# Optimization experiments

Measured on AMD Instinct MI355X. Metric: run time of the kernel, lower is better.

The kernel has to match this reference:

```python
import math
import jax, jax.numpy as jnp
import numpy as np

B, N, F = 4, 2048, 128
H, D = 8, 128  # num_heads, out_dim per head (out_dim == in_dim for residual)
EPS = 1e-5
NEG = -1e30  # finite stand-in for -inf; exp(NEG - rowmax) == 0 for any valid row


def setup_inputs() -> dict:
    key = jax.random.key(0)
    ks = jax.random.split(key, 10)
    x = jax.random.normal(ks[0], (B, N, F), dtype=jnp.float32)
    # sparse-ish graph adjacency mask + active-node mask
    attn_mask = jax.random.bernoulli(ks[1], 0.05, (B, N, N))
    # ensure self loops so most rows are non-empty (isolated-node nan path still exercised via node_mask)
    eye = jnp.eye(N, dtype=bool)[None]
    attn_mask = attn_mask | eye
    node_mask = jax.random.bernoulli(ks[2], 0.9, (B, N))
    s = 1.0 / math.sqrt(F)
    Wq = jax.random.normal(ks[3], (F, H * D), dtype=jnp.float32) * s
    Wk = jax.random.normal(ks[4], (F, H * D), dtype=jnp.float32) * s
    Wv = jax.random.normal(ks[5], (F, H * D), dtype=jnp.float32) * s
    Wo = jax.random.normal(ks[6], (H * D, D), dtype=jnp.float32) * (1.0 / math.sqrt(H * D))
    bo = jnp.zeros((D,), dtype=jnp.float32)
    gamma = jnp.ones((D,), dtype=jnp.float32)
    beta = jnp.zeros((D,), dtype=jnp.float32)
    return {"x": x, "attn_mask": attn_mask, "node_mask": node_mask,
            "Wq": Wq, "Wk": Wk, "Wv": Wv, "Wo": Wo, "bo": bo,
            "gamma": gamma, "beta": beta}


def reference(x, attn_mask, node_mask, Wq, Wk, Wv, Wo, bo, gamma, beta):
    # projections -> [B, H, N, D]
    q = (x @ Wq).reshape(B, N, H, D).transpose(0, 2, 1, 3)
    k = (x @ Wk).reshape(B, N, H, D).transpose(0, 2, 1, 3)
    v = (x @ Wv).reshape(B, N, H, D).transpose(0, 2, 1, 3)
    scores = jnp.einsum("bhnd,bhmd->bhnm", q, k) / math.sqrt(D)
    # pair_mask: adjacency (broadcast over heads) AND query-node validity
    pair_mask = attn_mask[:, None, :, :] & node_mask[:, None, :, None]  # [B,H(=1),N,N]
    scores = jnp.where(pair_mask, scores, NEG)
    attn = jax.nn.softmax(scores, axis=-1)
    # rows with no valid key (== torch's nan_to_num of all -inf softmax) -> zeros
    row_valid = pair_mask.any(axis=-1, keepdims=True)
    attn = jnp.where(row_valid, attn, 0.0)
    out = jnp.einsum("bhnm,bhmd->bhnd", attn, v)
    out = out.transpose(0, 2, 1, 3).reshape(B, N, H * D)
    out = out @ Wo + bo
    out = out + x  # residual (in_dim == out_dim)
    # LayerNorm over last dim
    mu = out.mean(axis=-1, keepdims=True)
    var = ((out - mu) ** 2).mean(axis=-1, keepdims=True)
    out = (out - mu) * jax.lax.rsqrt(var + EPS) * gamma + beta
    out = out * jax.nn.sigmoid(out)  # SiLU
    out = out * node_mask[..., None]
    return out
```

## Files before the change

kernel.cpp:

```cpp
#include <hip/hip_runtime.h>

#define NTOK 2048
#define NB 4
#define NH 8
#define DH 128

typedef __bf16 bf16x8 __attribute__((ext_vector_type(8)));
typedef unsigned short u16x8 __attribute__((ext_vector_type(8)));
typedef float f32x4 __attribute__((ext_vector_type(4)));
typedef float f32x16 __attribute__((ext_vector_type(16)));
typedef unsigned int u32x4 __attribute__((ext_vector_type(4)));

__device__ __forceinline__ f32x4 mfma16(bf16x8 a, bf16x8 b, f32x4 c) {
  return __builtin_amdgcn_mfma_f32_16x16x32_bf16(a, b, c, 0, 0, 0);
}
__device__ __forceinline__ f32x16 mfma32(bf16x8 a, bf16x8 b, f32x16 c) {
  return __builtin_amdgcn_mfma_f32_32x32x16_bf16(a, b, c, 0, 0, 0);
}
__device__ __forceinline__ bf16x8 ldb(const unsigned short* p) {
  return __builtin_bit_cast(bf16x8, *(const u16x8*)p);
}
__device__ __forceinline__ bf16x8 ldsb(const char* p) {
  return __builtin_bit_cast(bf16x8, *(const u16x8*)p);
}
__device__ __forceinline__ unsigned short f2bf(float f) {
  unsigned int u = __builtin_bit_cast(unsigned int, f);
  u += 0x7fffu + ((u >> 16) & 1u);
  return (unsigned short)(u >> 16);
}
__device__ __forceinline__ unsigned int cvtpk(float lo, float hi) {
  unsigned int r;
  asm("v_cvt_pk_bf16_f32 %0, %1, %2" : "=v"(r) : "v"(lo), "v"(hi));
  return r;
}
#if __has_builtin(__builtin_amdgcn_exp2f)
__device__ __forceinline__ float exp2a(float x) { return __builtin_amdgcn_exp2f(x); }
#else
__device__ __forceinline__ float exp2a(float x) { return __expf(x * 0.6931471805599453f); }
#endif
#define GLL(gsrc, ldst) __builtin_amdgcn_global_load_lds(                      \
    (const __attribute__((address_space(1))) void*)(gsrc),                     \
    (__attribute__((address_space(3))) void*)(ldst), 16, 0, 0)
#define WAITVM_(N) asm volatile("s_waitcnt vmcnt(" #N ")" ::: "memory")
#define WAITVM(N) WAITVM_(N)
#define SFENCE() asm volatile("" ::: "memory")

__device__ __forceinline__ bool mask_at(const void* p, int flag, int idx) {
  if (flag == 1) return ((const unsigned char*)p)[idx] != 0;
  return ((const int*)p)[idx] != 0;
}

__global__ __launch_bounds__(256) void k_prep(
    const float* __restrict__ x, const float* __restrict__ Wq,
    const float* __restrict__ Wk, const float* __restrict__ Wv,
    const float* __restrict__ Wo, const unsigned int* __restrict__ amdw,
    unsigned short* __restrict__ xb, unsigned short* __restrict__ wqt,
    unsigned short* __restrict__ wkt, unsigned short* __restrict__ wvt,
    unsigned short* __restrict__ wot, int* __restrict__ flag) {
  int bid = blockIdx.x, tid = threadIdx.x;
  if (bid == 0) {
    __shared__ int su8, sf32;
    if (tid == 0) { su8 = 0; sf32 = 0; }
    __syncthreads();
    const uint4* dw4 = (const uint4*)amdw;
    int lu8 = 0, lf32 = 0;
#pragma unroll
    for (int j = 0; j < 16; j++) {
      uint4 q = dw4[tid + j * 256];
      unsigned int vv[4] = {q.x, q.y, q.z, q.w};
#pragma unroll
      for (int e = 0; e < 4; e++) {
        unsigned int v = vv[e];
        if (v == 0x3f800000u) lf32 = 1;
        else if (v != 0u && v != 1u) lu8 = 1;
      }
    }
    if (lu8) atomicOr(&su8, 1);
    if (lf32) atomicOr(&sf32, 1);
    __syncthreads();
    if (tid == 0) *flag = sf32 ? 2 : (su8 ? 1 : 0);
    return;
  }
  if (bid < 513) {
    int base = (bid - 1) * 2048 + tid * 8;
    const float4* xf = (const float4*)(x + base);
    float4 a = xf[0], b = xf[1];
    u16x8 o;
    o[0] = f2bf(a.x); o[1] = f2bf(a.y); o[2] = f2bf(a.z); o[3] = f2bf(a.w);
    o[4] = f2bf(b.x); o[5] = f2bf(b.y); o[6] = f2bf(b.z); o[7] = f2bf(b.w);
    *(u16x8*)(xb + base) = o;
    return;
  }
  __shared__ float tile[64][65];
  int tb = bid - 513;
  int msel = tb >> 5, tt = tb & 31;
  const float* w; unsigned short* wt; int R, C;
  if (msel == 0)      { w = Wq; wt = wqt; R = 128;  C = 1024; }
  else if (msel == 1) { w = Wk; wt = wkt; R = 128;  C = 1024; }
  else if (msel == 2) { w = Wv; wt = wvt; R = 128;  C = 1024; }
  else                { w = Wo; wt = wot; R = 1024; C = 128; }
  int nrt = R >> 6;
  int rt = (tt % nrt) << 6, ct = (tt / nrt) << 6;
  {
    int cl = tid & 63, rg = tid >> 6;
#pragma unroll
    for (int j = 0; j < 16; j++) {
      int row = rg * 16 + j;
      tile[row][cl] = w[(size_t)(rt + row) * C + ct + cl];
    }
  }
  __syncthreads();
  {
    int rl = tid & 63, cg = tid >> 6;
#pragma unroll
    for (int j = 0; j < 16; j++) {
      int col = cg * 16 + j;
      wt[(size_t)(ct + col) * R + rt + rl] = f2bf(tile[rl][col]);
    }
  }
}

__global__ __launch_bounds__(256) void k_qkv_pack(
    const unsigned short* __restrict__ xb, const unsigned short* __restrict__ wqt,
    const unsigned short* __restrict__ wkt, const unsigned short* __restrict__ wvt,
    unsigned short* __restrict__ qb, unsigned short* __restrict__ kbuf,
    unsigned short* __restrict__ vtb, const void* __restrict__ am,
    const int* __restrict__ flagp, unsigned int* __restrict__ bits) {
  __shared__ char smem[49152];
  int bid = blockIdx.x;
  int lane = threadIdx.x & 63, w = threadIdx.x >> 6;
  if (bid >= 3072) {
    int flag = *flagp;
    size_t ebase = (size_t)(bid - 3072) * 8192 + (size_t)threadIdx.x * 32;
    unsigned int word = 0;
    if (flag == 1) {
      const uint4* p4 = (const uint4*)((const unsigned char*)am + ebase);
      uint4 q0 = p4[0], q1 = p4[1];
      unsigned int dw[8] = {q0.x, q0.y, q0.z, q0.w, q1.x, q1.y, q1.z, q1.w};
#pragma unroll
      for (int d = 0; d < 8; d++) {
        unsigned int v = dw[d];
        if (v & 0x000000FFu) word |= 1u << (d * 4 + 0);
        if (v & 0x0000FF00u) word |= 1u << (d * 4 + 1);
        if (v & 0x00FF0000u) word |= 1u << (d * 4 + 2);
        if (v & 0xFF000000u) word |= 1u << (d * 4 + 3);
      }
    } else {
      const uint4* p4 = (const uint4*)((const int*)am + ebase);
#pragma unroll
      for (int k = 0; k < 8; k++) {
        uint4 q = p4[k];
        if (q.x) word |= 1u << (k * 4 + 0);
        if (q.y) word |= 1u << (k * 4 + 1);
        if (q.z) word |= 1u << (k * 4 + 2);
        if (q.w) word |= 1u << (k * 4 + 3);
      }
    }
    bits[ebase >> 5] = word;
    return;
  }
  int which = bid >> 10;
  int rem = bid & 1023;
  int bx = rem & 127, by = rem >> 7;
  const unsigned short* wt = which == 0 ? wqt : (which == 1 ? wkt : wvt);
  int lo = lane & 15, g = lane >> 4;
  int rbase = bx * 64 + w * 16;
  int colb = by * 128;
  char* wl = smem;
  {
    const char* Wg = (const char*)(wt + (size_t)colb * 128);
#pragma unroll
    for (int s = 0; s < 8; s++) {
      int a = s * 4096 + w * 1024 + lane * 16;
      int r = a >> 8;
      int cb = (a & 255) ^ ((r & 7) << 4);
      GLL(Wg + r * 256 + cb, wl + s * 4096 + w * 1024);
    }
  }
  bf16x8 af[4];
  const unsigned short* xrow = xb + (size_t)(rbase + lo) * 128 + g * 8;
#pragma unroll
  for (int s = 0; s < 4; s++) af[s] = ldb(xrow + 32 * s);
  __syncthreads();
  f32x4 acc[8] = {};
  int xw = (lo & 7) << 4;
#pragma unroll
  for (int c = 0; c < 8; c++) {
    const char* wrow = wl + (c * 16 + lo) * 256;
#pragma unroll
    for (int s = 0; s < 4; s++)
      acc[c] = mfma16(af[s], ldsb(wrow + ((64 * s + 16 * g) ^ xw)), acc[c]);
  }
  if (which != 2) {
    float sc = (which == 0) ? 0.12751743f : 1.0f;
#pragma unroll
    for (int c = 0; c < 8; c++) {
#pragma unroll
      for (int r = 0; r < 4; r++) {
        int row = rbase + 4 * g + r;
        int col = colb + c * 16 + lo;
        int b = row >> 11, n = row & (NTOK - 1);
        int h = col >> 7, d = col & 127;
        unsigned short val = f2bf(acc[c][r] * sc);
        size_t bh = (size_t)(b * NH + h);
        if (which == 0) qb[(bh * NTOK + n) * DH + d] = val;
        else            kbuf[(bh * NTOK + n) * DH + d] = val;
      }
    }
    return;
  }
  unsigned short* vt_lds = (unsigned short*)(smem + 32768);
#pragma unroll
  for (int c = 0; c < 8; c++) {
#pragma unroll
    for (int r = 0; r < 4; r++) {
      int nl = w * 16 + 4 * g + r;
      int d = c * 16 + lo;
      int boff = d * 128 + ((nl * 2) ^ ((d & 7) << 4));
      *(unsigned short*)((char*)vt_lds + boff) = f2bf(acc[c][r]);
    }
  }
  __syncthreads();
  int t = threadIdx.x;
  int d = t >> 1, half = t & 1;
  int bb = (bx * 64) >> 11;
  int n0 = (bx * 64) & (NTOK - 1);
  size_t bh = (size_t)(bb * NH + by);
  unsigned short* dst = vtb + (bh * DH + d) * NTOK + n0 + half * 32;
  const char* srcb = (const char*)vt_lds + d * 128;
#pragma unroll
  for (int s = 0; s < 4; s++) {
    int lb = (half * 64 + s * 16) ^ ((d & 7) << 4);
    *(u16x8*)(dst + s * 8) = *(const u16x8*)(srcb + lb);
  }
}

__device__ __forceinline__ void stageK(const char* Kg, char* kl, int w, int lane) {
#pragma unroll
  for (int s = 0; s < 4; s++) {
    int a = s * 4096 + w * 1024 + lane * 16;
    int r = a >> 8;
    int cb = (a & 255) ^ ((r & 7) << 4);
    GLL(Kg + r * 256 + cb, kl + s * 4096 + w * 1024);
  }
}
__device__ __forceinline__ void stageV(const char* Vg, char* vl, int w, int lane) {
#pragma unroll
  for (int s = 0; s < 4; s++) {
    int a = s * 4096 + w * 1024 + lane * 16;
    int r = a >> 7;
    int cb = (a & 127) ^ ((r & 7) << 4);
    GLL(Vg + (size_t)r * (NTOK * 2) + cb, vl + s * 4096 + w * 1024);
  }
}

#define QKBLK(SC0, SC1, KC)                                                    \
  {                                                                            \
    _Pragma("unroll") for (int r_ = 0; r_ < 16; r_++) { SC0[r_] = 0.f; SC1[r_] = 0.f; } \
    const char* kr0_ = (KC) + ql * 256;                                        \
    const char* kr1_ = (KC) + (32 + ql) * 256;                                 \
    _Pragma("unroll")                                                          \
    for (int s_ = 0; s_ < 8; s_++) {                                           \
      int cb_ = (32 * s_ + 16 * hi) ^ xk;                                      \
      SC0 = mfma32(ldsb(kr0_ + cb_), qf[s_], SC0);                             \
      SC1 = mfma32(ldsb(kr1_ + cb_), qf[s_], SC1);                             \
    }                                                                          \
  }

#define SOFTPACK(SC0, SC1, MMV, PSV, FA0, FA1, FB0, FB1)                       \
  {                                                                            \
    unsigned int mw0_ = (MMV).x >> (4 * hi), mw1_ = (MMV).y >> (4 * hi);       \
    float sv0_[16], sv1_[16];                                                  \
    _Pragma("unroll")                                                          \
    for (int r_ = 0; r_ < 16; r_++) {                                          \
      int cp_ = (r_ & 3) + 8 * (r_ >> 2);                                      \
      sv0_[r_] = ((mw0_ >> cp_) & 1u) ? SC0[r_] : -3.0e38f;                    \
      sv1_[r_] = ((mw1_ >> cp_) & 1u) ? SC1[r_] : -3.0e38f;                    \
    }                                                                          \
    PSV = 0.f;                                                                 \
    _Pragma("unroll")                                                          \
    for (int r_ = 0; r_ < 16; r_++) { sv0_[r_] = exp2a(sv0_[r_] - m); PSV += sv0_[r_]; } \
    _Pragma("unroll")                                                          \
    for (int r_ = 0; r_ < 16; r_++) { sv1_[r_] = exp2a(sv1_[r_] - m); PSV += sv1_[r_]; } \
    unsigned int w8a_[8], w8b_[8], pa_[8], pb_[8];                             \
    _Pragma("unroll")                                                          \
    for (int j_ = 0; j_ < 8; j_++) {                                           \
      w8a_[j_] = cvtpk(sv0_[2 * j_], sv0_[2 * j_ + 1]);                        \
      w8b_[j_] = cvtpk(sv1_[2 * j_], sv1_[2 * j_ + 1]);                        \
    }                                                                          \
    _Pragma("unroll")                                                          \
    for (int j_ = 0; j_ < 8; j_++) {                                           \
      pa_[j_] = __shfl_xor((int)w8a_[j_], 32, 64);                             \
      pb_[j_] = __shfl_xor((int)w8b_[j_], 32, 64);                             \
    }                                                                          \
    u32x4 ta0_, ta1_, tb0_, tb1_;                                              \
    if (hi) {                                                                  \
      ta0_ = u32x4{pa_[2], pa_[3], w8a_[2], w8a_[3]};                          \
      ta1_ = u32x4{pa_[6], pa_[7], w8a_[6], w8a_[7]};                          \
      tb0_ = u32x4{pb_[2], pb_[3], w8b_[2], w8b_[3]};                          \
      tb1_ = u32x4{pb_[6], pb_[7], w8b_[6], w8b_[7]};                          \
    } else {                                                                   \
      ta0_ = u32x4{w8a_[0], w8a_[1], pa_[0], pa_[1]};                          \
      ta1_ = u32x4{w8a_[4], w8a_[5], pa_[4], pa_[5]};                          \
      tb0_ = u32x4{w8b_[0], w8b_[1], pb_[0], pb_[1]};                          \
      tb1_ = u32x4{w8b_[4], w8b_[5], pb_[4], pb_[5]};                          \
    }                                                                          \
    FA0 = __builtin_bit_cast(bf16x8, ta0_);                                    \
    FA1 = __builtin_bit_cast(bf16x8, ta1_);                                    \
    FB0 = __builtin_bit_cast(bf16x8, tb0_);                                    \
    FB1 = __builtin_bit_cast(bf16x8, tb1_);                                    \
  }

#define PVBLK(FA0, FA1, FB0, FB1, VC)                                          \
  {                                                                            \
    const char* vr0_ = (VC) + (ql + 0) * 128;                                  \
    const char* vr1_ = (VC) + (ql + 32) * 128;                                 \
    const char* vr2_ = (VC) + (ql + 64) * 128;                                 \
    const char* vr3_ = (VC) + (ql + 96) * 128;                                 \
    int c0_ = (16 * hi) ^ xk, c1_ = (32 + 16 * hi) ^ xk;                       \
    int c2_ = (64 + 16 * hi) ^ xk, c3_ = (96 + 16 * hi) ^ xk;                  \
    o0 = mfma32(FA0, ldsb(vr0_ + c0_), o0);                                    \
    o1 = mfma32(FA0, ldsb(vr1_ + c0_), o1);                                    \
    o2 = mfma32(FA0, ldsb(vr2_ + c0_), o2);                                    \
    o3 = mfma32(FA0, ldsb(vr3_ + c0_), o3);                                    \
    o0 = mfma32(FA1, ldsb(vr0_ + c1_), o0);                                    \
    o1 = mfma32(FA1, ldsb(vr1_ + c1_), o1);                                    \
    o2 = mfma32(FA1, ldsb(vr2_ + c1_), o2);                                    \
    o3 = mfma32(FA1, ldsb(vr3_ + c1_), o3);                                    \
    o0 = mfma32(FB0, ldsb(vr0_ + c2_), o0);                                    \
    o1 = mfma32(FB0, ldsb(vr1_ + c2_), o1);                                    \
    o2 = mfma32(FB0, ldsb(vr2_ + c2_), o2);                                    \
    o3 = mfma32(FB0, ldsb(vr3_ + c2_), o3);                                    \
    o0 = mfma32(FB1, ldsb(vr0_ + c3_), o0);                                    \
    o1 = mfma32(FB1, ldsb(vr1_ + c3_), o1);                                    \
    o2 = mfma32(FB1, ldsb(vr2_ + c3_), o2);                                    \
    o3 = mfma32(FB1, ldsb(vr3_ + c3_), o3);                                    \
  }

#define BIG(PSV)                                                               \
  if (__any((PSV) > 65536.0f)) {                                               \
    const float c_ = 1.52587890625e-05f;                                       \
    m += 16.0f; l *= c_;                                                       \
    _Pragma("unroll")                                                          \
    for (int r_ = 0; r_ < 16; r_++) { o0[r_] *= c_; o1[r_] *= c_; o2[r_] *= c_; o3[r_] *= c_; } \
  }

#define BODY(PI0, PI1, PI2, PI3, PSI, PO0, PO1, PO2, PO3, PSO, MMV)            \
  {                                                                            \
    __builtin_amdgcn_s_setprio(1);                                             \
    QKBLK(sT0, sT1, smem + ko_rd);                                             \
    PVBLK(PI0, PI1, PI2, PI3, smem + vo_pv);                                   \
    __builtin_amdgcn_s_setprio(0);                                             \
    l += PSI;                                                                  \
    BIG(PSI);                                                                  \
    SOFTPACK(sT0, sT1, MMV, PSO, PO0, PO1, PO2, PO3);                          \
  }

#define ROT_V() { int t_ = vo_pv; vo_pv = vo_mid; vo_mid = vo_st; vo_st = t_; }
#define SWAP_K() { int t_ = ko_rd; ko_rd = ko_nx; ko_nx = t_; }

#define TAIL(KT, VT, MMREG, MI)                                                \
  __builtin_amdgcn_s_barrier();                                                \
  stageK(Kbase + (size_t)(KT) * 16384, smem + ko_rd, w, lane);                 \
  stageV(Vbase + (size_t)(VT) * 128, smem + vo_st, w, lane);                   \
  SFENCE();                                                                    \
  MMREG = mrow[MI];                                                            \
  SFENCE();                                                                    \
  SWAP_K();                                                                    \
  ROT_V();

__global__ __launch_bounds__(256, 2) void k_attn64(
    const unsigned short* __restrict__ qb, const unsigned short* __restrict__ kbuf,
    const unsigned short* __restrict__ vtb, const unsigned int* __restrict__ mbits,
    unsigned short* __restrict__ aout) {
  __shared__ char smem[81920];
  int bid = blockIdx.x;
  int low3 = bid & 7, mid2 = (bid >> 3) & 3, qc = bid >> 5;
  int b = low3 >> 1, h = ((low3 & 1) << 2) | mid2;
  int bh = b * 8 + h;
  int lane = threadIdx.x & 63, w = threadIdx.x >> 6;
  int ql = lane & 31, hi = lane >> 5;
  int q0 = qc * 128 + w * 32;
  const char* Kbase = (const char*)(kbuf + (size_t)bh * NTOK * DH);
  const char* Vbase = (const char*)(vtb + (size_t)bh * NTOK * DH);
  int xk = (ql & 7) << 4;

  bf16x8 qf[8];
  {
    const unsigned short* qrow = qb + (size_t)bh * NTOK * DH + (size_t)(q0 + ql) * DH + 8 * hi;
#pragma unroll
    for (int s = 0; s < 8; s++) qf[s] = ldb(qrow + 16 * s);
  }
  const uint2* mrow = (const uint2*)(mbits + (size_t)b * (NTOK * NTOK / 32) + (size_t)(q0 + ql) * (NTOK / 32));
  SFENCE();
  uint2 mmB = mrow[0];
  uint2 mmA = mrow[1];
  SFENCE();
  stageK(Kbase, smem + 0, w, lane);
  stageK(Kbase + 16384, smem + 16384, w, lane);
  stageV(Vbase, smem + 32768, w, lane);
  SFENCE();

  int ko_rd = 0, ko_nx = 16384;
  int vo_pv = 65536, vo_mid = 32768, vo_st = 49152;
  f32x16 o0 = {}, o1 = {}, o2 = {}, o3 = {};
  f32x16 sT0, sT1;
  bf16x8 pE0, pE1, pE2, pE3, pO0, pO1, pO2, pO3;
  float psE = 0.f, psO = 0.f;
  float m = 0.0f, l = 0.0f;

  WAITVM(8); __builtin_amdgcn_s_barrier();
  QKBLK(sT0, sT1, smem + ko_rd);
  SOFTPACK(sT0, sT1, mmB, psE, pE0, pE1, pE2, pE3);
  TAIL(2, 1, mmB, 2);
  for (int tt = 1; tt <= 27; tt += 2) {
    WAITVM(9); __builtin_amdgcn_s_barrier();
    BODY(pE0, pE1, pE2, pE3, psE, pO0, pO1, pO2, pO3, psO, mmA);
    TAIL(tt + 2, tt + 1, mmA, tt + 2);
    WAITVM(9); __builtin_amdgcn_s_barrier();
    BODY(pO0, pO1, pO2, pO3, psO, pE0, pE1, pE2, pE3, psE, mmB);
    TAIL(tt + 3, tt + 2, mmB, tt + 3);
  }
  WAITVM(9); __builtin_amdgcn_s_barrier();
  BODY(pE0, pE1, pE2, pE3, psE, pO0, pO1, pO2, pO3, psO, mmA);
  TAIL(31, 30, mmA, 31);
  WAITVM(9); __builtin_amdgcn_s_barrier();
  BODY(pO0, pO1, pO2, pO3, psO, pE0, pE1, pE2, pE3, psE, mmB);
  __builtin_amdgcn_s_barrier();
  stageV(Vbase + (size_t)31 * 128, smem + vo_st, w, lane);
  SFENCE();
  SWAP_K();
  ROT_V();
  WAITVM(4); __builtin_amdgcn_s_barrier();
  BODY(pE0, pE1, pE2, pE3, psE, pO0, pO1, pO2, pO3, psO, mmA);
  ROT_V();
  WAITVM(0); __builtin_amdgcn_s_barrier();
  PVBLK(pO0, pO1, pO2, pO3, smem + vo_pv);
  l += psO;
  float lj = l + __shfl_xor(l, 32, 64);
  float linv = lj > 0.f ? 1.0f / lj : 0.0f;
  float li[16];
#pragma unroll
  for (int r = 0; r < 16; r++) {
    int qr = (r & 3) + 8 * (r >> 2) + 4 * hi;
    li[r] = __shfl(linv, qr, 64);
  }
  unsigned short* obase = aout + (size_t)b * NTOK * (NH * DH) + (size_t)h * DH + ql;
#pragma unroll
  for (int r = 0; r < 16; r++) {
    int qn = q0 + (r & 3) + 8 * (r >> 2) + 4 * hi;
    unsigned short* op = obase + (size_t)qn * (NH * DH);
    op[0]  = f2bf(o0[r] * li[r]);
    op[32] = f2bf(o1[r] * li[r]);
    op[64] = f2bf(o2[r] * li[r]);
    op[96] = f2bf(o3[r] * li[r]);
  }
}

__global__ __launch_bounds__(256) void k_gemm3(
    const unsigned short* __restrict__ aout, const unsigned short* __restrict__ wot,
    const float* __restrict__ x, const float* __restrict__ bo,
    const float* __restrict__ gamma, const float* __restrict__ beta,
    const void* __restrict__ nmask, const int* __restrict__ flagp,
    float* __restrict__ out) {
  __shared__ float red[4][16][132];
  int flag = *flagp;
  int lane = threadIdx.x & 63, w = threadIdx.x >> 6;
  int lo = lane & 15, g = lane >> 4;
  int rowb = blockIdx.x * 16;
  int k0 = w * 256;
  f32x4 acc[8] = {};
  const unsigned short* arow = aout + (size_t)(rowb + lo) * 1024 + k0 + g * 8;
#pragma unroll
  for (int ks = 0; ks < 8; ks++) {
    bf16x8 af = ldb(arow + 32 * ks);
#pragma unroll
    for (int t = 0; t < 8; t++) {
      bf16x8 bf = ldb(wot + (size_t)(t * 16 + lo) * 1024 + k0 + g * 8 + 32 * ks);
      acc[t] = mfma16(af, bf, acc[t]);
    }
  }
#pragma unroll
  for (int t = 0; t < 8; t++)
#pragma unroll
    for (int r = 0; r < 4; r++) red[w][4 * g + r][t * 16 + lo] = acc[t][r];
  __syncthreads();
  int row = threadIdx.x >> 4, cg = threadIdx.x & 15;
  float y[8];
#pragma unroll
  for (int j = 0; j < 8; j++) {
    int col = cg * 8 + j;
    y[j] = red[0][row][col] + red[1][row][col] + red[2][row][col] + red[3][row][col]
         + bo[col] + x[(size_t)(rowb + row) * 128 + col];
  }
  float s = 0.f;
#pragma unroll
  for (int j = 0; j < 8; j++) s += y[j];
  s += __shfl_xor(s, 1, 64); s += __shfl_xor(s, 2, 64);
  s += __shfl_xor(s, 4, 64); s += __shfl_xor(s, 8, 64);
  float mu = s * 0.0078125f;
  float vs = 0.f;
#pragma unroll
  for (int j = 0; j < 8; j++) { float d = y[j] - mu; vs += d * d; }
  vs += __shfl_xor(vs, 1, 64); vs += __shfl_xor(vs, 2, 64);
  vs += __shfl_xor(vs, 4, 64); vs += __shfl_xor(vs, 8, 64);
  float rstd = rsqrtf(vs * 0.0078125f + 1e-5f);
  float nm = mask_at(nmask, flag, rowb + row) ? 1.0f : 0.0f;
  float ov[8];
#pragma unroll
  for (int j = 0; j < 8; j++) {
    int col = cg * 8 + j;
    float z = (y[j] - mu) * rstd * gamma[col] + beta[col];
    z = z / (1.0f + __expf(-z));
    ov[j] = z * nm;
  }
  float* op = out + (size_t)(rowb + row) * 128 + cg * 8;
  *(float4*)op = float4{ov[0], ov[1], ov[2], ov[3]};
  *(float4*)(op + 4) = float4{ov[4], ov[5], ov[6], ov[7]};
}

extern "C" void kernel_launch(void* const* d_in, const int* in_sizes, int n_in,
                              void* d_out, int out_size, void* d_ws, size_t ws_size,
                              hipStream_t stream) {
  (void)in_sizes; (void)n_in; (void)out_size;
  const float* x = (const float*)d_in[0];
  const void* amask = d_in[1];
  const void* nmask = d_in[2];
  const float* Wq = (const float*)d_in[3];
  const float* Wk = (const float*)d_in[4];
  const float* Wv = (const float*)d_in[5];
  const float* Wo = (const float*)d_in[6];
  const float* bo = (const float*)d_in[7];
  const float* gamma = (const float*)d_in[8];
  const float* beta = (const float*)d_in[9];
  float* out = (float*)d_out;
  char* ws = (char*)d_ws;

  constexpr size_t OFF_FLAG = 0;
  constexpr size_t OFF_XB   = 256;
  constexpr size_t OFF_WQT  = OFF_XB  + (size_t)8192 * 128 * 2;
  constexpr size_t OFF_WKT  = OFF_WQT + (size_t)1024 * 128 * 2;
  constexpr size_t OFF_WVT  = OFF_WKT + (size_t)1024 * 128 * 2;
  constexpr size_t OFF_WOT  = OFF_WVT + (size_t)1024 * 128 * 2;
  constexpr size_t OFF_BITS = OFF_WOT + (size_t)1024 * 128 * 2;
  constexpr size_t OFF_QB   = OFF_BITS + (size_t)NB * NTOK * NTOK / 8;
  constexpr size_t OFF_KB   = OFF_QB  + (size_t)NB * NH * NTOK * DH * 2;
  constexpr size_t OFF_VTB  = OFF_KB  + (size_t)NB * NH * NTOK * DH * 2;
  constexpr size_t OFF_AO   = OFF_VTB + (size_t)NB * NH * NTOK * DH * 2;
  constexpr size_t TOTAL    = OFF_AO  + (size_t)NB * NTOK * NH * DH * 2;
  if (ws_size < TOTAL) return;

  int* flag = (int*)(ws + OFF_FLAG);
  unsigned short* xb  = (unsigned short*)(ws + OFF_XB);
  unsigned short* wqt = (unsigned short*)(ws + OFF_WQT);
  unsigned short* wkt = (unsigned short*)(ws + OFF_WKT);
  unsigned short* wvt = (unsigned short*)(ws + OFF_WVT);
  unsigned short* wot = (unsigned short*)(ws + OFF_WOT);
  unsigned int* bits  = (unsigned int*)(ws + OFF_BITS);
  unsigned short* qb  = (unsigned short*)(ws + OFF_QB);
  unsigned short* kbf = (unsigned short*)(ws + OFF_KB);
  unsigned short* vtb = (unsigned short*)(ws + OFF_VTB);
  unsigned short* ao  = (unsigned short*)(ws + OFF_AO);

  k_prep<<<641, 256, 0, stream>>>(x, Wq, Wk, Wv, Wo, (const unsigned int*)amask,
                                  xb, wqt, wkt, wvt, wot, flag);
  k_qkv_pack<<<5120, 256, 0, stream>>>(xb, wqt, wkt, wvt, qb, kbf, vtb,
                                       amask, flag, bits);
  k_attn64<<<512, 256, 0, stream>>>(qb, kbf, vtb, bits, ao);
  k_gemm3<<<512, 256, 0, stream>>>(ao, wot, x, bo, gamma, beta, nmask, flag, out);
}
```

Baseline: 137.0 us.

## Split attention over key halves with partial outputs and a combine kernel

Adds a split-KV attention kernel that processes 32-key tiles over half of the key range per block, doubling the grid to 1024 blocks. Each block writes fp32 partial outputs plus row sums and running max to workspace, and a new combine kernel merges the two halves and writes bf16 attention output. The aim is higher occupancy and more parallelism on the attention stage. The cost is extra fp32 partial traffic (about 64 MB written and read) and one more launch. The new path only runs when the workspace is large enough.

```diff
diff --git a/kernel.cpp b/kernel.cpp
--- a/kernel.cpp
+++ b/kernel.cpp
@@ -233,6 +233,162 @@
     int lb = (half * 64 + s * 16) ^ ((d & 7) << 4);
     *(u16x8*)(dst + s * 8) = *(const u16x8*)(srcb + lb);
   }
+}
+
+__device__ __forceinline__ void stageK32(const char* Kg, char* kl, int w, int lane) {
+#pragma unroll
+  for (int s = 0; s < 2; s++) {
+    int a = s * 4096 + w * 1024 + lane * 16;
+    int r = a >> 8;
+    int cb = (a & 255) ^ ((r & 7) << 4);
+    GLL(Kg + r * 256 + cb, kl + s * 4096 + w * 1024);
+  }
+}
+__device__ __forceinline__ void stageV32(const char* Vg, char* vl, int w, int lane) {
+#pragma unroll
+  for (int s = 0; s < 2; s++) {
+    int a = s * 4096 + w * 1024 + lane * 16;
+    int r = a >> 6;
+    int cb = (a & 63) ^ ((r & 3) << 4);
+    GLL(Vg + (size_t)r * (NTOK * 2) + cb, vl + s * 4096 + w * 1024);
+  }
+}
+
+__global__ __launch_bounds__(256, 4) void k_attn32s(
+    const unsigned short* __restrict__ qb, const unsigned short* __restrict__ kbuf,
+    const unsigned short* __restrict__ vtb, const unsigned int* __restrict__ mbits,
+    float* __restrict__ opart, float* __restrict__ lpart, float* __restrict__ mpart) {
+  __shared__ char smem[32768];
+  int bid = blockIdx.x;
+  int low3 = bid & 7, mid2 = (bid >> 3) & 3, split = (bid >> 5) & 1, qc = bid >> 6;
+  int b = low3 >> 1, h = ((low3 & 1) << 2) | mid2;
+  int bh = b * 8 + h;
+  int lane = threadIdx.x & 63, w = threadIdx.x >> 6;
+  int ql = lane & 31, hi = lane >> 5;
+  int q0 = qc * 128 + w * 32;
+  const char* Kg = (const char*)(kbuf + (size_t)bh * NTOK * DH) + (size_t)split * 1024 * 256;
+  const char* Vg = (const char*)(vtb + (size_t)bh * NTOK * DH) + (size_t)split * 2048;
+  int xk = (ql & 7) << 4;
+  int xv = (ql & 3) << 4;
+
+  bf16x8 qf[8];
+  {
+    const unsigned short* qrow = qb + (size_t)bh * NTOK * DH + (size_t)(q0 + ql) * DH + 8 * hi;
+#pragma unroll
+    for (int s = 0; s < 8; s++) qf[s] = ldb(qrow + 16 * s);
+  }
+  const unsigned int* mrow = mbits + (size_t)b * (NTOK * NTOK / 32)
+                           + (size_t)(q0 + ql) * (NTOK / 32) + split * 32;
+  char* kl = smem;
+  char* vl = smem + 16384;
+  stageK32(Kg, kl, w, lane);
+  stageV32(Vg, vl, w, lane);
+  __syncthreads();
+
+  f32x16 o0 = {}, o1 = {}, o2 = {}, o3 = {};
+  float m = 0.0f, l = 0.0f;
+  for (int kt = 0; kt < 32; kt++) {
+    int cur = kt & 1;
+    const char* kc = kl + cur * 8192;
+    const char* vc = vl + cur * 8192;
+    if (kt < 31) {
+      stageK32(Kg + (size_t)(kt + 1) * 8192, kl + (1 - cur) * 8192, w, lane);
+      stageV32(Vg + (size_t)(kt + 1) * 64, vl + (1 - cur) * 8192, w, lane);
+    }
+    unsigned int mword = mrow[kt];
+    f32x16 sT = {};
+    const char* kr = kc + ql * 256;
+#pragma unroll
+    for (int s = 0; s < 8; s++)
+      sT = mfma32(ldsb(kr + ((32 * s + 16 * hi) ^ xk)), qf[s], sT);
+    unsigned int mw = mword >> (4 * hi);
+    float sv[16];
+#pragma unroll
+    for (int r = 0; r < 16; r++) {
+      int cp = (r & 3) + 8 * (r >> 2);
+      sv[r] = ((mw >> cp) & 1u) ? sT[r] : -3.0e38f;
+    }
+    float ps = 0.f;
+#pragma unroll
+    for (int r = 0; r < 16; r++) { sv[r] = exp2a(sv[r] - m); ps += sv[r]; }
+    ps += __shfl_xor(ps, 32, 64);
+    l += ps;
+    unsigned int w8[8], pa[8];
+#pragma unroll
+    for (int j = 0; j < 8; j++) w8[j] = cvtpk(sv[2 * j], sv[2 * j + 1]);
+#pragma unroll
+    for (int j = 0; j < 8; j++) pa[j] = __shfl_xor((int)w8[j], 32, 64);
+    u32x4 t0, t1;
+    if (hi) {
+      t0 = u32x4{pa[2], pa[3], w8[2], w8[3]};
+      t1 = u32x4{pa[6], pa[7], w8[6], w8[7]};
+    } else {
+      t0 = u32x4{w8[0], w8[1], pa[0], pa[1]};
+      t1 = u32x4{w8[4], w8[5], pa[4], pa[5]};
+    }
+    bf16x8 fk0 = __builtin_bit_cast(bf16x8, t0);
+    bf16x8 fk1 = __builtin_bit_cast(bf16x8, t1);
+    {
+      const char* vr0 = vc + (ql + 0) * 64;
+      const char* vr1 = vc + (ql + 32) * 64;
+      const char* vr2 = vc + (ql + 64) * 64;
+      const char* vr3 = vc + (ql + 96) * 64;
+      int c0 = (16 * hi) ^ xv, c1 = (32 + 16 * hi) ^ xv;
+      o0 = mfma32(fk0, ldsb(vr0 + c0), o0);
+      o1 = mfma32(fk0, ldsb(vr1 + c0), o1);
+      o2 = mfma32(fk0, ldsb(vr2 + c0), o2);
+      o3 = mfma32(fk0, ldsb(vr3 + c0), o3);
+      o0 = mfma32(fk1, ldsb(vr0 + c1), o0);
+      o1 = mfma32(fk1, ldsb(vr1 + c1), o1);
+      o2 = mfma32(fk1, ldsb(vr2 + c1), o2);
+      o3 = mfma32(fk1, ldsb(vr3 + c1), o3);
+    }
+    if (__any(ps > 65536.0f)) {
+      const float c = 1.52587890625e-05f;
+      m += 16.0f; l *= c;
+#pragma unroll
+      for (int r = 0; r < 16; r++) { o0[r] *= c; o1[r] *= c; o2[r] *= c; o3[r] *= c; }
+    }
+    __syncthreads();
+  }
+  size_t prow = (size_t)split * (32 * NTOK) + (size_t)bh * NTOK;
+#pragma unroll
+  for (int r = 0; r < 16; r++) {
+    int q = q0 + (r & 3) + 8 * (r >> 2) + 4 * hi;
+    float* op = opart + (prow + q) * 128;
+    op[ql]      = o0[r];
+    op[32 + ql] = o1[r];
+    op[64 + ql] = o2[r];
+    op[96 + ql] = o3[r];
+  }
+  if (hi == 0) {
+    lpart[prow + q0 + ql] = l;
+    mpart[prow + q0 + ql] = m;
+  }
+}
+
+__global__ __launch_bounds__(256) void k_comb(
+    const float* __restrict__ opart, const float* __restrict__ lpart,
+    const float* __restrict__ mpart, unsigned short* __restrict__ aout) {
+  int idx = blockIdx.x * 256 + threadIdx.x;
+  int d4 = idx & 31;
+  int row = idx >> 5;
+  float l0 = lpart[row], l1 = lpart[65536 + row];
+  float m0 = mpart[row], m1 = mpart[65536 + row];
+  float M = fmaxf(m0, m1);
+  float w0 = exp2a(m0 - M), w1 = exp2a(m1 - M);
+  float den = l0 * w0 + l1 * w1;
+  float inv = den > 0.f ? 1.0f / den : 0.f;
+  float4 a = *((const float4*)(opart + (size_t)row * 128) + d4);
+  float4 c = *((const float4*)(opart + ((size_t)65536 + row) * 128) + d4);
+  ushort4 r;
+  r.x = f2bf((a.x * w0 + c.x * w1) * inv);
+  r.y = f2bf((a.y * w0 + c.y * w1) * inv);
+  r.z = f2bf((a.z * w0 + c.z * w1) * inv);
+  r.w = f2bf((a.w * w0 + c.w * w1) * inv);
+  int bh = row >> 11, q = row & (NTOK - 1);
+  int b = bh >> 3, h = bh & 7;
+  *(ushort4*)(aout + ((size_t)(b * NTOK + q) * 1024) + h * 128 + d4 * 4) = r;
 }
 
 __device__ __forceinline__ void stageK(const char* Kg, char* kl, int w, int lane) {
@@ -548,7 +704,12 @@
   constexpr size_t OFF_VTB  = OFF_KB  + (size_t)NB * NH * NTOK * DH * 2;
   constexpr size_t OFF_AO   = OFF_VTB + (size_t)NB * NH * NTOK * DH * 2;
   constexpr size_t TOTAL    = OFF_AO  + (size_t)NB * NTOK * NH * DH * 2;
+  constexpr size_t OFF_OP   = TOTAL;
+  constexpr size_t OFF_LP   = OFF_OP + (size_t)2 * 32 * NTOK * 128 * 4;
+  constexpr size_t OFF_MP   = OFF_LP + (size_t)2 * 32 * NTOK * 4;
+  constexpr size_t TOTAL2   = OFF_MP + (size_t)2 * 32 * NTOK * 4;
   if (ws_size < TOTAL) return;
+  bool use_split = ws_size >= TOTAL2;
 
   int* flag = (int*)(ws + OFF_FLAG);
   unsigned short* xb  = (unsigned short*)(ws + OFF_XB);
@@ -561,11 +722,19 @@
   unsigned short* kbf = (unsigned short*)(ws + OFF_KB);
   unsigned short* vtb = (unsigned short*)(ws + OFF_VTB);
   unsigned short* ao  = (unsigned short*)(ws + OFF_AO);
+  float* opart = (float*)(ws + OFF_OP);
+  float* lpart = (float*)(ws + OFF_LP);
+  float* mpart = (float*)(ws + OFF_MP);
 
   k_prep<<<641, 256, 0, stream>>>(x, Wq, Wk, Wv, Wo, (const unsigned int*)amask,
                                   xb, wqt, wkt, wvt, wot, flag);
   k_qkv_pack<<<5120, 256, 0, stream>>>(xb, wqt, wkt, wvt, qb, kbf, vtb,
                                        amask, flag, bits);
-  k_attn64<<<512, 256, 0, stream>>>(qb, kbf, vtb, bits, ao);
+  if (use_split) {
+    k_attn32s<<<1024, 256, 0, stream>>>(qb, kbf, vtb, bits, opart, lpart, mpart);
+    k_comb<<<8192, 256, 0, stream>>>(opart, lpart, mpart, ao);
+  } else {
+    k_attn64<<<512, 256, 0, stream>>>(qb, kbf, vtb, bits, ao);
+  }
   k_gemm3<<<512, 256, 0, stream>>>(ao, wot, x, bo, gamma, beta, nmask, flag, out);
 }
```

Result: slower. 216.9 us (+58.3%).
